# Optimization experiments

Measured on AMD Instinct MI355X. Metric: run time of the kernel, lower is better.

The kernel has to match this reference:

```python
import jax, jax.numpy as jnp
import numpy as np

D = 64        # kg_embedding_dim
T = 4096      # tokens
N = 20000     # kg nodes
M = T + N     # total nodes
E = 100000    # edges
R = 50        # relation types (num_edge_embeddings)
V = 100000    # num_node_embeddings
TOK = 768     # token_embedding_size


def setup_inputs() -> dict:
    key = jax.random.key(0)
    ks = jax.random.split(key, 24)
    s = 0.05
    node_ids = jax.random.randint(ks[0], (N,), 0, V)
    edge_index = jax.random.randint(ks[1], (2, E), 0, M)
    rel_ids = jax.random.randint(ks[2], (E,), 0, R)
    edge_attr = jax.nn.one_hot(rel_ids, R, dtype=jnp.float32)  # [E,R]
    token_embeddings = jax.random.normal(ks[3], (T, TOK), dtype=jnp.float32)
    node_type_labels = jax.random.randint(ks[4], (M,), 0, 3)
    return {
        'node_ids': node_ids,
        'edge_index': edge_index,
        'edge_attr': edge_attr,
        'token_embeddings': token_embeddings,
        'node_type_labels': node_type_labels,
        # learned params
        'kg_emb': jax.random.normal(ks[5], (V, D), dtype=jnp.float32) * s,
        'rel_emb': jax.random.normal(ks[6], (R, D), dtype=jnp.float32) * s,
        'w_e2': jax.random.normal(ks[7], (D, D * D), dtype=jnp.float32) * s,
        'b_e2': jnp.zeros((D * D,), dtype=jnp.float32),
        'att1_w': jax.random.normal(ks[8], (2 * D, 1), dtype=jnp.float32) * s,
        'att1_b': jnp.zeros((1,), dtype=jnp.float32),
        'root1': jax.random.normal(ks[9], (D, D), dtype=jnp.float32) * s,
        'bias1': jnp.zeros((D,), dtype=jnp.float32),
        'att2_w': jax.random.normal(ks[10], (2 * D, 1), dtype=jnp.float32) * s,
        'att2_b': jnp.zeros((1,), dtype=jnp.float32),
        'root2': jax.random.normal(ks[11], (D, D), dtype=jnp.float32) * s,
        'bias2': jnp.zeros((D,), dtype=jnp.float32),
        'w_lin1': jax.random.normal(ks[12], (TOK, D), dtype=jnp.float32) * s,
        'b_lin1': jnp.zeros((D,), dtype=jnp.float32),
        'w_lin2': jax.random.normal(ks[13], (D, TOK), dtype=jnp.float32) * s,
        'b_lin2': jnp.zeros((TOK,), dtype=jnp.float32),
        'w_nt': jax.random.normal(ks[14], (D, 3), dtype=jnp.float32) * s,
        'b_nt': jnp.zeros((3,), dtype=jnp.float32),
    }


def _ecgat(x, src, dst, w_edge, att_w, att_b, root, bias):
    # x: [M,D], w_edge: [E,D,D]
    x_j = x[src]                                    # gather source nodes [E,D]
    x_i = x[dst]                                    # gather target nodes [E,D]
    nbr = jnp.einsum('ed,edo->eo', x_j, w_edge)     # per-edge matmul [E,D]
    a = jnp.concatenate([x_i, nbr], axis=1) @ att_w + att_b   # [E,1]
    a = jax.nn.softmax(a, axis=0)                   # global softmax over edges (dim=0 in torch)
    msg = x_j * a                                   # message = x_j * alpha
    aggr = jax.ops.segment_sum(msg, dst, num_segments=M)      # scatter-add [M,D]
    return aggr + x @ root + bias


def reference(node_ids, edge_index, edge_attr, token_embeddings, node_type_labels,
              kg_emb, rel_emb, w_e2, b_e2,
              att1_w, att1_b, root1, bias1,
              att2_w, att2_b, root2, bias2,
              w_lin1, b_lin1, w_lin2, b_lin2, w_nt, b_nt):
    src, dst = edge_index[0], edge_index[1]
    tok = token_embeddings @ w_lin1 + b_lin1        # [T,D]
    nodes = kg_emb[node_ids]                        # [N,D]
    x = jnp.concatenate([tok, nodes], axis=0)       # [M,D]

    # EdgeNet (shared by both conv layers, same edge_attr -> compute once)
    e_emb = edge_attr @ rel_emb                     # [E,D]
    w_edge = jax.nn.relu(e_emb @ w_e2 + b_e2).reshape(E, D, D)  # [E,D,D]

    x1 = _ecgat(x, src, dst, w_edge, att1_w, att1_b, root1, bias1)
    h = jax.nn.relu(x1)                             # dropout = identity in eval
    final_x = _ecgat(h, src, dst, w_edge, att2_w, att2_b, root2, bias2)

    # link_pred loss (MSE, masked, mean over all elements)
    pred_tails = final_x[src] + e_emb
    edge_labels = final_x[dst]
    mask = (edge_attr[:, -3:].sum(axis=1) == 0).astype(final_x.dtype)[:, None]
    kge_loss = jnp.mean((pred_tails - edge_labels) ** 2 * mask)

    # node-type classification loss (cross entropy)
    logp = jax.nn.log_softmax(final_x @ w_nt + b_nt, axis=-1)
    nt_loss = -jnp.mean(jnp.take_along_axis(logp, node_type_labels[:, None], axis=1))

    final_outputs = final_x @ w_lin2 + b_lin2       # [M,TOK]
    return final_outputs, kge_loss, nt_loss
```

## Files before the change

kernel.cpp:

```cpp
#include <hip/hip_runtime.h>

#define Dd   64
#define Tt   4096
#define Nn   20000
#define Mm   24096
#define Ee   100000
#define Rr   50
#define TOK  768

#define NB_TOK   512
#define NB_NODES 1250
#define NB_RELID 4883
#define NB_W     800
#define NB_ZERO  95
#define NBM_HIST 391
#define NBM_U    13
#define NBM_P    6024
#define NBA_FILL 391
#define NBA_ATT  2048
#define NKGE     391
#define NNT      95
#define NFIN     (NKGE+NNT)
#define NGROW    189
#define NGCOL    6
#define NGEMMT   (NGROW*NGCOL)

__device__ __forceinline__ float waveRed(float v){
  #pragma unroll
  for(int o=32;o;o>>=1) v += __shfl_xor(v,o,64);
  return v;
}

__global__ __launch_bounds__(256) void k_prep(
    const float* __restrict__ A, const float* __restrict__ wl1, const float* __restrict__ bl1,
    const int* __restrict__ ids, const float* __restrict__ kg,
    const float* __restrict__ ea, int* __restrict__ relid,
    const float* __restrict__ rel, const float* __restrict__ w2, const float* __restrict__ b2,
    float* __restrict__ W, int* __restrict__ deg, float* __restrict__ S,
    float* __restrict__ x){
  __shared__ float As[8*TOK];
  int b = blockIdx.x;
  const int t = threadIdx.x, lane = t&63, wave = t>>6;
  if(b < NB_TOK){
    const int rbase = b*8;
    #pragma unroll
    for(int i=0;i<6;i++){
      int f = t + 256*i;
      int row = f/192, c4 = (f - row*192)*4;
      *(float4*)&As[row*TOK + c4] = *(const float4*)&A[(size_t)(rbase+row)*TOK + c4];
    }
    __syncthreads();
    const int r0 = wave*2, r1 = r0+1;
    float a0=bl1[lane], a1=a0, c0=0.f, c1=0.f;
    for(int k=0;k<TOK;k+=2){
      float w0 = wl1[(size_t)k*Dd + lane];
      float w1 = wl1[(size_t)(k+1)*Dd + lane];
      a0 += As[r0*TOK+k]*w0;  c0 += As[r0*TOK+k+1]*w1;
      a1 += As[r1*TOK+k]*w0;  c1 += As[r1*TOK+k+1]*w1;
    }
    x[(size_t)(rbase+r0)*Dd + lane] = a0+c0;
    x[(size_t)(rbase+r1)*Dd + lane] = a1+c1;
  } else if(b < NB_TOK+NB_NODES){
    int tt = (b-NB_TOK)*256 + t;
    int i = tt>>4, c = tt&15;
    ((float4*)x)[(size_t)(Tt+i)*16 + c] = ((const float4*)kg)[(size_t)ids[i]*16 + c];
  } else if(b < NB_TOK+NB_NODES+NB_RELID){
    int tt = (b-NB_TOK-NB_NODES)*256 + t;
    size_t g4 = (size_t)tt*4;
    if(g4 < (size_t)Ee*Rr){
      float4 v = *(const float4*)&ea[g4];
      #pragma unroll
      for(int j=0;j<4;j++){
        if(((const float*)&v)[j] > 0.5f){
          unsigned g = (unsigned)(g4 + j);
          unsigned e = g / 50u;
          relid[e] = (int)(g - e*50u);
        }
      }
    }
  } else if(b < NB_TOK+NB_NODES+NB_RELID+NB_W){
    int tt = (b-NB_TOK-NB_NODES-NB_RELID)*256 + t;
    int r = tt>>12, j = tt&4095;
    float acc = b2[j];
    const float* rp = rel + r*Dd;
    #pragma unroll 8
    for(int d=0;d<Dd;d++) acc += rp[d] * w2[(size_t)d*4096 + j];
    W[tt] = acc > 0.f ? acc : 0.f;
  } else {
    int tt = (b-NB_TOK-NB_NODES-NB_RELID-NB_W)*256 + t;
    if(tt < Mm) deg[tt] = 0;
    else if(tt < Mm+8) S[tt-Mm] = 0.f;
  }
}

__global__ __launch_bounds__(256) void k_mid(const int* __restrict__ ei,
    int* __restrict__ deg, const float* __restrict__ W,
    const float* __restrict__ a1w, const float* __restrict__ a2w,
    float* __restrict__ U1, float* __restrict__ U2,
    const float* __restrict__ x, float* __restrict__ p){
  int b = blockIdx.x;
  const int t = threadIdx.x, lane = t&63, wave = t>>6;
  if(b < NBM_HIST){
    int e = b*256 + t;
    if(e < Ee) atomicAdd(&deg[ei[Ee+e]], 1);
  } else if(b < NBM_HIST+NBM_U){
    int tt = (b-NBM_HIST)*256 + t;
    if(tt < Rr*Dd){
      const float* wp = W + (size_t)(tt>>6)*4096 + (size_t)(tt&63)*Dd;
      float s1 = 0.f, s2 = 0.f;
      #pragma unroll 8
      for(int o=0;o<Dd;o++){ float w = wp[o]; s1 += w*a1w[Dd+o]; s2 += w*a2w[Dd+o]; }
      U1[tt] = s1; U2[tt] = s2;
    }
  } else {
    int i = (b-NBM_HIST-NBM_U)*4 + wave;
    float pv = waveRed(x[(size_t)i*Dd + lane] * a1w[lane]);
    if(lane==0) p[i] = pv;
  }
}

__global__ __launch_bounds__(1024) void k_scan(const int* __restrict__ deg,
    int* __restrict__ rowptr, int* __restrict__ cursor){
  __shared__ int ts[1024];
  int t = threadIdx.x;
  int base = t*24;
  int loc[24];
  int s = 0;
  #pragma unroll
  for(int j=0;j<24;j++){
    int idx = base+j;
    int d = (idx < Mm) ? deg[idx] : 0;
    loc[j] = s; s += d;
  }
  ts[t] = s;
  __syncthreads();
  for(int off=1; off<1024; off<<=1){
    int add = (t>=off) ? ts[t-off] : 0;
    __syncthreads();
    ts[t] += add;
    __syncthreads();
  }
  int excl = ts[t] - s;
  #pragma unroll
  for(int j=0;j<24;j++){
    int idx = base+j;
    if(idx < Mm){ int v = excl + loc[j]; rowptr[idx] = v; cursor[idx] = v; }
  }
  if(t==1023) rowptr[Mm] = ts[1023];
}

__global__ __launch_bounds__(256) void k_attf(const float* __restrict__ x,
    const int* __restrict__ ei, const int* __restrict__ relid,
    const float* __restrict__ U, const float* __restrict__ p,
    const float* __restrict__ ab, float* __restrict__ expa, float* __restrict__ S,
    int* __restrict__ cursor, int* __restrict__ eidx,
    int dorelu, int dofill){
  __shared__ float sw[4];
  int b = blockIdx.x;
  if(dofill){
    if(b < NBA_FILL){
      int e = b*256 + threadIdx.x;
      if(e < Ee){
        int d = ei[Ee+e];
        int pos = atomicAdd(&cursor[d], 1);
        eidx[pos] = e;
      }
      return;
    }
    b -= NBA_FILL;
  }
  int lane = threadIdx.x&63, wid = threadIdx.x>>6;
  int gw = b*4 + wid;
  float ab0 = ab[0];
  float acc = 0.f;
  for(int e = gw; e < Ee; e += 4*NBA_ATT){
    int src = ei[e], dst = ei[Ee+e], r = relid[e];
    float xv = x[(size_t)src*Dd + lane];
    if(dorelu) xv = fmaxf(xv, 0.f);
    float v = waveRed(xv * U[r*Dd + lane]);
    float ex = expf(v + p[dst] + ab0);
    if(lane==0) expa[e] = ex;
    acc += ex;
  }
  if(lane==0) sw[wid] = acc;
  __syncthreads();
  if(threadIdx.x==0) atomicAdd(S, sw[0]+sw[1]+sw[2]+sw[3]);
}

__global__ __launch_bounds__(256) void k_aggr(const float* __restrict__ x,
    const int* __restrict__ ei, const int* __restrict__ rowptr,
    const int* __restrict__ eidx, const float* __restrict__ expa,
    const float* __restrict__ S, const float* __restrict__ root,
    const float* __restrict__ bias, const float* __restrict__ awn,
    float* __restrict__ y, float* __restrict__ pnext, int dorelu){
  int lane = threadIdx.x&63, wid = threadIdx.x>>6;
  int dst = blockIdx.x*4 + wid;
  float invS = 1.f / S[0];
  int j0 = rowptr[dst], j1 = rowptr[dst+1];
  int deg = j1 - j0;
  float acc = 0.f;
  for(int base=0; base<deg; base+=64){
    int rem = deg - base;
    int n = rem < 64 ? rem : 64;
    float a = 0.f; int src = 0;
    if(lane < n){
      int e = eidx[j0 + base + lane];
      a = expa[e];
      src = ei[e];
    }
    for(int c=0; c<n; c+=8){
      float aj[8]; float xv[8];
      #pragma unroll
      for(int k=0;k<8;k++){
        int sj = __shfl(src, c+k, 64);
        aj[k]  = __shfl(a,   c+k, 64);
        xv[k]  = x[(size_t)sj*Dd + lane];
      }
      #pragma unroll
      for(int k=0;k<8;k++){
        float v = xv[k];
        if(dorelu) v = fmaxf(v, 0.f);
        acc += aj[k]*v;
      }
    }
  }
  acc *= invS;
  float xd = x[(size_t)dst*Dd + lane];
  if(dorelu) xd = fmaxf(xd, 0.f);
  float rsum = bias[lane];
  #pragma unroll 16
  for(int k=0;k<Dd;k++){
    float xk = __shfl(xd, k, 64);
    rsum += xk * root[k*Dd + lane];
  }
  float o = acc + rsum;
  y[(size_t)dst*Dd + lane] = o;
  if(pnext){
    float orl = fmaxf(o, 0.f);
    float pv = waveRed(orl * awn[lane]);
    if(lane==0) pnext[dst] = pv;
  }
}

__global__ __launch_bounds__(256) void k_out(const float* __restrict__ fx,
    const float* __restrict__ w, const float* __restrict__ b,
    const int* __restrict__ ei, const int* __restrict__ relid,
    const float* __restrict__ rel, const int* __restrict__ lab,
    const float* __restrict__ wnt, const float* __restrict__ bnt,
    float* __restrict__ S, float* __restrict__ out){
  __shared__ float aT[Dd][132];
  __shared__ float ws[Dd][128];
  if(blockIdx.x < NGEMMT){
    const int bb = blockIdx.x;
    const int cg = bb / NGROW;
    const int bx = bb - cg*NGROW;
    const int t = threadIdx.x;
    const int r0 = bx*128, co = cg*128;
    #pragma unroll
    for(int i=0;i<8;i++){
      int f = t + 256*i;
      int r = f>>4, k4 = (f&15)*4;
      float4 v = *(const float4*)&fx[(size_t)(r0+r)*Dd + k4];
      aT[k4+0][r]=v.x; aT[k4+1][r]=v.y; aT[k4+2][r]=v.z; aT[k4+3][r]=v.w;
    }
    #pragma unroll
    for(int i=0;i<8;i++){
      int f = t + 256*i;
      int kk = f>>5, c4 = (f&31)*4;
      *(float4*)&ws[kk][c4] = *(const float4*)&w[(size_t)kk*TOK + co + c4];
    }
    __syncthreads();
    const int tr = t>>4, tc = t&15;
    const int rb = tr*8, cb = tc*4;
    float4 bv0 = *(const float4*)&b[co+cb];
    float4 bv1 = *(const float4*)&b[co+64+cb];
    float acc[8][8];
    #pragma unroll
    for(int i=0;i<8;i++){
      acc[i][0]=bv0.x; acc[i][1]=bv0.y; acc[i][2]=bv0.z; acc[i][3]=bv0.w;
      acc[i][4]=bv1.x; acc[i][5]=bv1.y; acc[i][6]=bv1.z; acc[i][7]=bv1.w;
    }
    #pragma unroll 4
    for(int k=0;k<Dd;k++){
      float4 a0 = *(const float4*)&aT[k][rb];
      float4 a1 = *(const float4*)&aT[k][rb+4];
      float4 w0 = *(const float4*)&ws[k][cb];
      float4 w1 = *(const float4*)&ws[k][cb+64];
      float av[8] = {a0.x,a0.y,a0.z,a0.w,a1.x,a1.y,a1.z,a1.w};
      float wv[8] = {w0.x,w0.y,w0.z,w0.w,w1.x,w1.y,w1.z,w1.w};
      #pragma unroll
      for(int i=0;i<8;i++){
        #pragma unroll
        for(int j=0;j<8;j++) acc[i][j] += av[i]*wv[j];
      }
    }
    #pragma unroll
    for(int i=0;i<8;i++){
      int row = r0 + rb + i;
      if(row < Mm){
        float4 o0; o0.x=acc[i][0]; o0.y=acc[i][1]; o0.z=acc[i][2]; o0.w=acc[i][3];
        float4 o1; o1.x=acc[i][4]; o1.y=acc[i][5]; o1.z=acc[i][6]; o1.w=acc[i][7];
        *(float4*)&out[(size_t)row*TOK + co + cb] = o0;
        *(float4*)&out[(size_t)row*TOK + co + 64 + cb] = o1;
      }
    }
    return;
  }
  {
    __shared__ float sr[4];
    const int lb2 = blockIdx.x - NGEMMT;
    const int t = threadIdx.x, lane = t&63, wid = t>>6;
    float acc = 0.f;
    int slot;
    if(lb2 < NKGE){
      slot = 2;
      const int cb = (lb2*4 + wid)*64;
      int e = cb + lane;
      bool vld = e < Ee;
      int sv = vld ? ei[e]    : 0;
      int dv = vld ? ei[Ee+e] : 0;
      int rv = vld ? relid[e] : 47;
      #pragma unroll 8
      for(int j=0;j<64;j++){
        int r = __shfl(rv, j, 64);
        int s = __shfl(sv, j, 64);
        int d = __shfl(dv, j, 64);
        float m = (r < 47) ? 1.f : 0.f;
        float diff = fx[(size_t)s*Dd + lane] + rel[r*Dd + lane] - fx[(size_t)d*Dd + lane];
        acc += m*diff*diff;
      }
      acc = waveRed(acc);
    } else {
      slot = 3;
      int i = (lb2 - NKGE)*256 + t;
      float contrib = 0.f;
      if(i < Mm){
        const float* r = fx + (size_t)i*Dd;
        float l0 = bnt[0], l1 = bnt[1], l2 = bnt[2];
        #pragma unroll 8
        for(int k=0;k<Dd;k++){
          float f = r[k];
          l0 += f*wnt[k*3+0]; l1 += f*wnt[k*3+1]; l2 += f*wnt[k*3+2];
        }
        float mx = fmaxf(l0, fmaxf(l1,l2));
        float lse = logf(expf(l0-mx)+expf(l1-mx)+expf(l2-mx)) + mx;
        int lb = lab[i];
        float lp = (lb==0 ? l0 : (lb==1 ? l1 : l2)) - lse;
        contrib = -lp;
      }
      acc = waveRed(contrib);
    }
    if(lane==0) sr[wid] = acc;
    __syncthreads();
    if(t==0){
      atomicAdd(&S[slot], sr[0]+sr[1]+sr[2]+sr[3]);
      __threadfence();
      int prev = atomicAdd((int*)&S[4], 1);
      if(prev == NFIN-1){
        float v2 = atomicAdd(&S[2], 0.f);
        float v3 = atomicAdd(&S[3], 0.f);
        size_t base = (size_t)Mm*TOK;
        out[base+0] = v2 / (float)(Ee*Dd);
        out[base+1] = v3 / (float)Mm;
      }
    }
  }
}

extern "C" void kernel_launch(void* const* d_in, const int* in_sizes, int n_in,
                              void* d_out, int out_size, void* d_ws, size_t ws_size,
                              hipStream_t stream) {
  const int*   node_ids = (const int*)d_in[0];
  const int*   ei       = (const int*)d_in[1];
  const float* eattr    = (const float*)d_in[2];
  const float* tokemb   = (const float*)d_in[3];
  const int*   labels   = (const int*)d_in[4];
  const float* kg       = (const float*)d_in[5];
  const float* rel      = (const float*)d_in[6];
  const float* w_e2     = (const float*)d_in[7];
  const float* b_e2     = (const float*)d_in[8];
  const float* a1w      = (const float*)d_in[9];
  const float* a1b      = (const float*)d_in[10];
  const float* root1    = (const float*)d_in[11];
  const float* bias1    = (const float*)d_in[12];
  const float* a2w      = (const float*)d_in[13];
  const float* a2b      = (const float*)d_in[14];
  const float* root2    = (const float*)d_in[15];
  const float* bias2    = (const float*)d_in[16];
  const float* wlin1    = (const float*)d_in[17];
  const float* blin1    = (const float*)d_in[18];
  const float* wlin2    = (const float*)d_in[19];
  const float* blin2    = (const float*)d_in[20];
  const float* wnt      = (const float*)d_in[21];
  const float* bnt      = (const float*)d_in[22];

  float* wsb = (float*)d_ws;
  float* x    = wsb;
  float* h    = x  + (size_t)Mm*Dd;
  float* fx   = h  + (size_t)Mm*Dd;
  float* W    = fx + (size_t)Mm*Dd;
  float* U1   = W  + Rr*4096;
  float* U2   = U1 + Rr*Dd;
  float* expa = U2 + Rr*Dd;
  float* p    = expa + Ee;
  float* S    = p + Mm;
  int* relid  = (int*)(S + 8);
  int* deg    = relid + Ee;
  int* rowptr = deg + Mm;
  int* cursor = rowptr + Mm + 1;
  int* eidx   = cursor + Mm;
  float* out  = (float*)d_out;

  k_prep<<<NB_TOK+NB_NODES+NB_RELID+NB_W+NB_ZERO, 256, 0, stream>>>(
      tokemb, wlin1, blin1, node_ids, kg, eattr, relid, rel, w_e2, b_e2, W, deg, S, x);
  k_mid <<<NBM_HIST+NBM_U+NBM_P, 256, 0, stream>>>(ei, deg, W, a1w, a2w, U1, U2, x, p);
  k_scan<<<1, 1024, 0, stream>>>(deg, rowptr, cursor);

  k_attf<<<NBA_FILL+NBA_ATT, 256, 0, stream>>>(x, ei, relid, U1, p, a1b, expa, S,
                                               cursor, eidx, 0, 1);
  k_aggr<<<Mm/4, 256, 0, stream>>>(x, ei, rowptr, eidx, expa, S, root1, bias1, a2w, h, p, 0);

  k_attf<<<NBA_ATT, 256, 0, stream>>>(h, ei, relid, U2, p, a2b, expa, S+1,
                                      (int*)0, (int*)0, 1, 0);
  k_aggr<<<Mm/4, 256, 0, stream>>>(h, ei, rowptr, eidx, expa, S+1, root2, bias2,
                                   (const float*)0, fx, (float*)0, 1);

  k_out <<<NGEMMT + NFIN, 256, 0, stream>>>(
      fx, wlin2, blin2, ei, relid, rel, labels, wnt, bnt, S, out);
}
```

Before: 388.0 us.

## Precompute per-node relation attention scores to replace per-edge dot products

Instead of computing a 64-wide dot product per edge (x[src]·U[rel]) with one wave per edge, the change precomputes Y[node][rel] = x[node]·U[rel] for all 50 relations plus the p term in one node-wise pass. The per-edge attention kernel then becomes a single gather from Y with one thread per edge. The node-level Y computation is fused into the scan launch for layer 1 and placed in a new kernel for layer 2, and the p computation is removed from k_mid and k_aggr. This trades 100k wave-wide reductions for a 24k×50 node-level product and an extra launch, and it reuses the fx buffer as scratch for Y.

```diff
diff --git a/kernel.cpp b/kernel.cpp
--- a/kernel.cpp
+++ b/kernel.cpp
@@ -15,9 +15,9 @@
 #define NB_ZERO  95
 #define NBM_HIST 391
 #define NBM_U    13
-#define NBM_P    6024
+#define NSCAN_Y  1506
 #define NBA_FILL 391
-#define NBA_ATT  2048
+#define NBA_ATT  391
 #define NKGE     391
 #define NNT      95
 #define NFIN     (NKGE+NNT)
@@ -96,14 +96,13 @@
 __global__ __launch_bounds__(256) void k_mid(const int* __restrict__ ei,
     int* __restrict__ deg, const float* __restrict__ W,
     const float* __restrict__ a1w, const float* __restrict__ a2w,
-    float* __restrict__ U1, float* __restrict__ U2,
-    const float* __restrict__ x, float* __restrict__ p){
+    float* __restrict__ U1, float* __restrict__ U2){
   int b = blockIdx.x;
-  const int t = threadIdx.x, lane = t&63, wave = t>>6;
+  const int t = threadIdx.x;
   if(b < NBM_HIST){
     int e = b*256 + t;
     if(e < Ee) atomicAdd(&deg[ei[Ee+e]], 1);
-  } else if(b < NBM_HIST+NBM_U){
+  } else {
     int tt = (b-NBM_HIST)*256 + t;
     if(tt < Rr*Dd){
       const float* wp = W + (size_t)(tt>>6)*4096 + (size_t)(tt&63)*Dd;
@@ -112,54 +111,93 @@
       for(int o=0;o<Dd;o++){ float w = wp[o]; s1 += w*a1w[Dd+o]; s2 += w*a2w[Dd+o]; }
       U1[tt] = s1; U2[tt] = s2;
     }
-  } else {
-    int i = (b-NBM_HIST-NBM_U)*4 + wave;
-    float pv = waveRed(x[(size_t)i*Dd + lane] * a1w[lane]);
-    if(lane==0) p[i] = pv;
   }
 }
 
 __global__ __launch_bounds__(1024) void k_scan(const int* __restrict__ deg,
-    int* __restrict__ rowptr, int* __restrict__ cursor){
+    int* __restrict__ rowptr, int* __restrict__ cursor,
+    const float* __restrict__ x, const float* __restrict__ U1,
+    const float* __restrict__ a1w, float* __restrict__ Y, float* __restrict__ p){
   __shared__ int ts[1024];
+  __shared__ float UT[Dd][64];
   int t = threadIdx.x;
-  int base = t*24;
-  int loc[24];
-  int s = 0;
-  #pragma unroll
-  for(int j=0;j<24;j++){
-    int idx = base+j;
-    int d = (idx < Mm) ? deg[idx] : 0;
-    loc[j] = s; s += d;
-  }
-  ts[t] = s;
+  if(blockIdx.x == 0){
+    int base = t*24;
+    int loc[24];
+    int s = 0;
+    #pragma unroll
+    for(int j=0;j<24;j++){
+      int idx = base+j;
+      int d = (idx < Mm) ? deg[idx] : 0;
+      loc[j] = s; s += d;
+    }
+    ts[t] = s;
+    __syncthreads();
+    for(int off=1; off<1024; off<<=1){
+      int add = (t>=off) ? ts[t-off] : 0;
+      __syncthreads();
+      ts[t] += add;
+      __syncthreads();
+    }
+    int excl = ts[t] - s;
+    #pragma unroll
+    for(int j=0;j<24;j++){
+      int idx = base+j;
+      if(idx < Mm){ int v = excl + loc[j]; rowptr[idx] = v; cursor[idx] = v; }
+    }
+    if(t==1023) rowptr[Mm] = ts[1023];
+    return;
+  }
+  for(int idx=t; idx<Rr*Dd; idx+=1024) UT[idx&63][idx>>6] = U1[idx];
+  if(t < Dd){ UT[t][50] = a1w[t]; UT[t][51] = 0.f; }
   __syncthreads();
-  for(int off=1; off<1024; off<<=1){
-    int add = (t>=off) ? ts[t-off] : 0;
-    __syncthreads();
-    ts[t] += add;
-    __syncthreads();
-  }
-  int excl = ts[t] - s;
-  #pragma unroll
-  for(int j=0;j<24;j++){
-    int idx = base+j;
-    if(idx < Mm){ int v = excl + loc[j]; rowptr[idx] = v; cursor[idx] = v; }
-  }
-  if(t==1023) rowptr[Mm] = ts[1023];
-}
-
-__global__ __launch_bounds__(256) void k_attf(const float* __restrict__ x,
+  const int lane = t&63, wave = t>>6;
+  const int i = (blockIdx.x-1)*16 + wave;
+  float xv = x[(size_t)i*Dd + lane];
+  float acc = 0.f;
+  int cl = lane < 51 ? lane : 51;
+  #pragma unroll 8
+  for(int k=0;k<Dd;k++){
+    float xk = __shfl(xv, k, 64);
+    acc += xk * UT[k][cl];
+  }
+  if(lane < 50) Y[(size_t)i*50 + lane] = acc;
+  else if(lane == 50) p[i] = acc;
+}
+
+__global__ __launch_bounds__(256) void k_y2(const float* __restrict__ h,
+    const float* __restrict__ U2, const float* __restrict__ a2w,
+    float* __restrict__ Y, float* __restrict__ p){
+  __shared__ float UT[Dd][64];
+  const int t = threadIdx.x;
+  for(int idx=t; idx<Rr*Dd; idx+=256) UT[idx&63][idx>>6] = U2[idx];
+  if(t < Dd){ UT[t][50] = a2w[t]; UT[t][51] = 0.f; }
+  __syncthreads();
+  const int lane = t&63, wave = t>>6;
+  const int i = blockIdx.x*4 + wave;
+  float xv = fmaxf(h[(size_t)i*Dd + lane], 0.f);
+  float acc = 0.f;
+  int cl = lane < 51 ? lane : 51;
+  #pragma unroll 8
+  for(int k=0;k<Dd;k++){
+    float xk = __shfl(xv, k, 64);
+    acc += xk * UT[k][cl];
+  }
+  if(lane < 50) Y[(size_t)i*50 + lane] = acc;
+  else if(lane == 50) p[i] = acc;
+}
+
+__global__ __launch_bounds__(256) void k_attf(const float* __restrict__ Y,
     const int* __restrict__ ei, const int* __restrict__ relid,
-    const float* __restrict__ U, const float* __restrict__ p,
-    const float* __restrict__ ab, float* __restrict__ expa, float* __restrict__ S,
-    int* __restrict__ cursor, int* __restrict__ eidx,
-    int dorelu, int dofill){
-  __shared__ float sw[4];
+    const float* __restrict__ p, const float* __restrict__ ab,
+    float* __restrict__ expa, float* __restrict__ S,
+    int* __restrict__ cursor, int* __restrict__ eidx, int dofill){
+  __shared__ float sr[4];
   int b = blockIdx.x;
+  const int t = threadIdx.x, lane = t&63, wid = t>>6;
   if(dofill){
     if(b < NBA_FILL){
-      int e = b*256 + threadIdx.x;
+      int e = b*256 + t;
       if(e < Ee){
         int d = ei[Ee+e];
         int pos = atomicAdd(&cursor[d], 1);
@@ -169,30 +207,24 @@
     }
     b -= NBA_FILL;
   }
-  int lane = threadIdx.x&63, wid = threadIdx.x>>6;
-  int gw = b*4 + wid;
-  float ab0 = ab[0];
-  float acc = 0.f;
-  for(int e = gw; e < Ee; e += 4*NBA_ATT){
+  int e = b*256 + t;
+  float ex = 0.f;
+  if(e < Ee){
     int src = ei[e], dst = ei[Ee+e], r = relid[e];
-    float xv = x[(size_t)src*Dd + lane];
-    if(dorelu) xv = fmaxf(xv, 0.f);
-    float v = waveRed(xv * U[r*Dd + lane]);
-    float ex = expf(v + p[dst] + ab0);
-    if(lane==0) expa[e] = ex;
-    acc += ex;
-  }
-  if(lane==0) sw[wid] = acc;
+    ex = expf(Y[(size_t)src*50 + r] + p[dst] + ab[0]);
+    expa[e] = ex;
+  }
+  float acc = waveRed(ex);
+  if(lane==0) sr[wid] = acc;
   __syncthreads();
-  if(threadIdx.x==0) atomicAdd(S, sw[0]+sw[1]+sw[2]+sw[3]);
+  if(t==0) atomicAdd(S, sr[0]+sr[1]+sr[2]+sr[3]);
 }
 
 __global__ __launch_bounds__(256) void k_aggr(const float* __restrict__ x,
     const int* __restrict__ ei, const int* __restrict__ rowptr,
     const int* __restrict__ eidx, const float* __restrict__ expa,
     const float* __restrict__ S, const float* __restrict__ root,
-    const float* __restrict__ bias, const float* __restrict__ awn,
-    float* __restrict__ y, float* __restrict__ pnext, int dorelu){
+    const float* __restrict__ bias, float* __restrict__ y, int dorelu){
   int lane = threadIdx.x&63, wid = threadIdx.x>>6;
   int dst = blockIdx.x*4 + wid;
   float invS = 1.f / S[0];
@@ -233,13 +265,7 @@
     float xk = __shfl(xd, k, 64);
     rsum += xk * root[k*Dd + lane];
   }
-  float o = acc + rsum;
-  y[(size_t)dst*Dd + lane] = o;
-  if(pnext){
-    float orl = fmaxf(o, 0.f);
-    float pv = waveRed(orl * awn[lane]);
-    if(lane==0) pnext[dst] = pv;
-  }
+  y[(size_t)dst*Dd + lane] = acc + rsum;
 }
 
 __global__ __launch_bounds__(256) void k_out(const float* __restrict__ fx,
@@ -409,21 +435,22 @@
   int* rowptr = deg + Mm;
   int* cursor = rowptr + Mm + 1;
   int* eidx   = cursor + Mm;
+  float* Y    = fx;
   float* out  = (float*)d_out;
 
   k_prep<<<NB_TOK+NB_NODES+NB_RELID+NB_W+NB_ZERO, 256, 0, stream>>>(
       tokemb, wlin1, blin1, node_ids, kg, eattr, relid, rel, w_e2, b_e2, W, deg, S, x);
-  k_mid <<<NBM_HIST+NBM_U+NBM_P, 256, 0, stream>>>(ei, deg, W, a1w, a2w, U1, U2, x, p);
-  k_scan<<<1, 1024, 0, stream>>>(deg, rowptr, cursor);
-
-  k_attf<<<NBA_FILL+NBA_ATT, 256, 0, stream>>>(x, ei, relid, U1, p, a1b, expa, S,
-                                               cursor, eidx, 0, 1);
-  k_aggr<<<Mm/4, 256, 0, stream>>>(x, ei, rowptr, eidx, expa, S, root1, bias1, a2w, h, p, 0);
-
-  k_attf<<<NBA_ATT, 256, 0, stream>>>(h, ei, relid, U2, p, a2b, expa, S+1,
-                                      (int*)0, (int*)0, 1, 0);
-  k_aggr<<<Mm/4, 256, 0, stream>>>(h, ei, rowptr, eidx, expa, S+1, root2, bias2,
-                                   (const float*)0, fx, (float*)0, 1);
+  k_mid <<<NBM_HIST+NBM_U, 256, 0, stream>>>(ei, deg, W, a1w, a2w, U1, U2);
+  k_scan<<<1+NSCAN_Y, 1024, 0, stream>>>(deg, rowptr, cursor, x, U1, a1w, Y, p);
+
+  k_attf<<<NBA_FILL+NBA_ATT, 256, 0, stream>>>(Y, ei, relid, p, a1b, expa, S,
+                                               cursor, eidx, 1);
+  k_aggr<<<Mm/4, 256, 0, stream>>>(x, ei, rowptr, eidx, expa, S, root1, bias1, h, 0);
+
+  k_y2  <<<Mm/4, 256, 0, stream>>>(h, U2, a2w, Y, p);
+  k_attf<<<NBA_ATT, 256, 0, stream>>>(Y, ei, relid, p, a2b, expa, S+1,
+                                      (int*)0, (int*)0, 0);
+  k_aggr<<<Mm/4, 256, 0, stream>>>(h, ei, rowptr, eidx, expa, S+1, root2, bias2, fx, 1);
 
   k_out <<<NGEMMT + NFIN, 256, 0, stream>>>(
       fx, wlin2, blin2, ei, relid, rel, labels, wnt, bnt, S, out);
```

New measurement: 389.6 us. No clear change (+0.4%).
